# Performance work log

Hardware: AMD Instinct MI355X
Metric: run time of the kernel (lower is better)

Reference implementation:

```python
import jax, jax.numpy as jnp
import numpy as np

N, D, C = 4096, 512, 64
MARGIN = 1.0
INF = jnp.float32(1e30)


def setup_inputs() -> dict:
    key = jax.random.key(0)
    k1, k2 = jax.random.split(key)
    embeddings = jax.random.normal(k1, (N, D), dtype=jnp.float32)
    targets = jax.random.randint(k2, (N,), 0, C)
    return {"embeddings": embeddings, "targets": targets}


def _triplet_loss(embeddings, targets, margin=MARGIN):
    # Squared pairwise distances [N, N] (differentiable, used for the loss)
    sq_norms = jnp.sum(embeddings * embeddings, axis=1)
    sq_dist = jnp.maximum(
        sq_norms[:, None] + sq_norms[None, :] - 2.0 * (embeddings @ embeddings.T), 0.0
    )
    # Euclidean distances for mining only (index selection is non-differentiable in torch)
    dist = jnp.sqrt(jax.lax.stop_gradient(sq_dist))

    same = targets[:, None] == targets[None, :]  # [N, N] same-label mask

    # Hardest negative per anchor: argmax_k (d_ap - d_ak + margin) == argmin_k d_ak over negatives
    neg_dist = jnp.where(same, INF, dist)
    n_idx = jnp.argmin(neg_dist, axis=1)   # [N] hardest negative index per anchor
    min_neg = jnp.min(neg_dist, axis=1)    # [N] its euclidean distance

    idx = jnp.arange(dist.shape[0])
    # anchor-positive pairs: same label, a < p (torch.combinations on sorted indices)
    pair_mask = same & (idx[:, None] < idx[None, :])
    # triplet kept only if mined loss (euclidean) strictly positive
    valid = pair_mask & (dist - min_neg[:, None] + margin > 0)

    ap_sq = sq_dist                         # [N, N] squared anchor-positive distances
    an_sq = sq_dist[idx, n_idx]             # [N]   squared anchor-hard-negative distances
    losses = jax.nn.relu(ap_sq - an_sq[:, None] + margin)

    cnt = jnp.sum(valid)
    denom = jnp.maximum(cnt, 1).astype(losses.dtype)
    loss = jnp.sum(jnp.where(valid, losses, 0.0)) / denom

    correct = jnp.sum(valid & (ap_sq < an_sq[:, None]))
    accuracy = correct.astype(jnp.float32) / jnp.maximum(cnt, 1).astype(jnp.float32)
    return loss, accuracy


def reference(embeddings, targets):
    return _triplet_loss(embeddings, targets)
```

## Files before the change

kernel.cpp:

```cpp
#include <hip/hip_runtime.h>

#define N 4096
#define D 512
#define MARGIN 1.0f
#define TILE 64
#define BK 64
#define SKB 144
#define NTILES (N / TILE)
#define NTRI (NTILES * (NTILES + 1) / 2)
#define FINF 3.0e38f

#define NSLOT 64
#define SLOTW 16

typedef __attribute__((ext_vector_type(8))) short short8;
typedef __attribute__((ext_vector_type(4))) float floatx4;

__device__ __forceinline__ unsigned short f2bf(float f) {
  unsigned int u = __float_as_uint(f);
  u += 0x7FFFu + ((u >> 16) & 1u);
  return (unsigned short)(u >> 16);
}

__global__ void init_kernel(unsigned int* __restrict__ an_sq_bits, unsigned int* __restrict__ accs) {
  int i = blockIdx.x * 256 + threadIdx.x;
  if (i < N) an_sq_bits[i] = 0x7F800000u;
  if (i < NSLOT * SLOTW) accs[i] = 0u;
}

__global__ __launch_bounds__(256) void prep_kernel(const float* __restrict__ E,
                                                   unsigned short* __restrict__ Ebf,
                                                   float* __restrict__ norms) {
  const int row = blockIdx.x;
  const int tid = threadIdx.x;
  const float2 v = reinterpret_cast<const float2*>(E + (size_t)row * D)[tid];
  float s = v.x * v.x + v.y * v.y;
  unsigned int packed = ((unsigned int)f2bf(v.y) << 16) | (unsigned int)f2bf(v.x);
  reinterpret_cast<unsigned int*>(Ebf + (size_t)row * D)[tid] = packed;
  for (int off = 32; off > 0; off >>= 1) s += __shfl_down(s, off);
  __shared__ float wsum[4];
  if ((tid & 63) == 0) wsum[tid >> 6] = s;
  __syncthreads();
  if (tid == 0) norms[row] = wsum[0] + wsum[1] + wsum[2] + wsum[3];
}

__global__ __launch_bounds__(256, 6) void gemm_min_kernel(const unsigned short* __restrict__ Ebf,
                                                          const float* __restrict__ norms,
                                                          const int* __restrict__ targets,
                                                          unsigned int* __restrict__ an_sq_bits) {
  const int u = blockIdx.x;
  int i = (int)((sqrtf(8.0f * (float)u + 1.0f) - 1.0f) * 0.5f);
  while ((i + 1) * (i + 2) / 2 <= u) ++i;
  while (i * (i + 1) / 2 > u) --i;
  const int tm = u - i * (i + 1) / 2;
  const int tn = i;

  __shared__ alignas(16) unsigned char As[TILE * SKB];
  __shared__ alignas(16) unsigned char Bs[TILE * SKB];
  __shared__ float s_rmin[2][TILE];
  __shared__ float s_cmin[2][TILE];

  const int tid = threadIdx.x;
  const int wave = tid >> 6, lane = tid & 63;
  const int quad = lane >> 4, l16 = lane & 15;
  const int wr = wave >> 1, wc = wave & 1;
  const int rowBase = tm * TILE, colBase = tn * TILE;

  floatx4 acc[2][2];
#pragma unroll
  for (int a = 0; a < 2; a++)
#pragma unroll
    for (int b = 0; b < 2; b++) acc[a][b] = (floatx4){0.f, 0.f, 0.f, 0.f};

  for (int k0 = 0; k0 < D; k0 += BK) {
#pragma unroll
    for (int s = tid; s < TILE * 8; s += 256) {
      const int r = s >> 3, q = s & 7;
      const uint4 va = *reinterpret_cast<const uint4*>(&Ebf[(size_t)(rowBase + r) * D + k0 + q * 8]);
      *reinterpret_cast<uint4*>(&As[r * SKB + q * 16]) = va;
      const uint4 vb = *reinterpret_cast<const uint4*>(&Ebf[(size_t)(colBase + r) * D + k0 + q * 8]);
      *reinterpret_cast<uint4*>(&Bs[r * SKB + q * 16]) = vb;
    }
    __syncthreads();
#pragma unroll
    for (int ks = 0; ks < 2; ks++) {
      short8 af[2], bf[2];
#pragma unroll
      for (int s = 0; s < 2; s++) {
        af[s] = *reinterpret_cast<const short8*>(&As[(wr * 32 + s * 16 + l16) * SKB + ks * 64 + quad * 16]);
        bf[s] = *reinterpret_cast<const short8*>(&Bs[(wc * 32 + s * 16 + l16) * SKB + ks * 64 + quad * 16]);
      }
#pragma unroll
      for (int sm = 0; sm < 2; sm++)
#pragma unroll
        for (int sn = 0; sn < 2; sn++)
          acc[sm][sn] = __builtin_amdgcn_mfma_f32_16x16x32_bf16(af[sm], bf[sn], acc[sm][sn], 0, 0, 0);
    }
    __syncthreads();
  }

  int tcol[2];
  float ncol[2];
#pragma unroll
  for (int sn = 0; sn < 2; sn++) {
    const int gc = colBase + wc * 32 + sn * 16 + l16;
    tcol[sn] = targets[gc];
    ncol[sn] = norms[gc];
  }
  float colmin[2] = {FINF, FINF};
#pragma unroll
  for (int sm = 0; sm < 2; sm++) {
#pragma unroll
    for (int r = 0; r < 4; r++) {
      const int rloc = wr * 32 + sm * 16 + quad * 4 + r;
      const int grow = rowBase + rloc;
      const int trow = targets[grow];
      const float nrow = norms[grow];
      float rowmin = FINF;
#pragma unroll
      for (int sn = 0; sn < 2; sn++) {
        const float sq = fmaxf(nrow + ncol[sn] - 2.0f * acc[sm][sn][r], 0.0f);
        if (tcol[sn] != trow) {
          rowmin = fminf(rowmin, sq);
          colmin[sn] = fminf(colmin[sn], sq);
        }
      }
#pragma unroll
      for (int off = 1; off < 16; off <<= 1) rowmin = fminf(rowmin, __shfl_xor(rowmin, off));
      if (l16 == 0) s_rmin[wc][rloc] = rowmin;
    }
  }
#pragma unroll
  for (int sn = 0; sn < 2; sn++) {
    float cm = colmin[sn];
    cm = fminf(cm, __shfl_xor(cm, 16));
    cm = fminf(cm, __shfl_xor(cm, 32));
    if (quad == 0) s_cmin[wr][wc * 32 + sn * 16 + l16] = cm;
  }
  __syncthreads();
  if (tid < TILE) {
    const float m = fminf(s_rmin[0][tid], s_rmin[1][tid]);
    if (m < FINF) atomicMin(&an_sq_bits[rowBase + tid], __float_as_uint(m));
  } else if (tid < 2 * TILE) {
    const int c = tid - TILE;
    const float m = fminf(s_cmin[0][c], s_cmin[1][c]);
    if (m < FINF) atomicMin(&an_sq_bits[colBase + c], __float_as_uint(m));
  }
}

__global__ __launch_bounds__(256) void loss_kernel(const float* __restrict__ E,
                                                   const int* __restrict__ targets,
                                                   const float* __restrict__ norms,
                                                   const unsigned int* __restrict__ an_sq_bits,
                                                   float* __restrict__ accs) {
  const int i = blockIdx.x;
  const int tid = threadIdx.x, wave = tid >> 6, lane = tid & 63;
  __shared__ int list[512];
  __shared__ int lcount;
  __shared__ float s_sum[4];
  __shared__ unsigned int s_cnt[4], s_cor[4];
  if (tid == 0) lcount = 0;
  __syncthreads();
  const int ti = targets[i];
  for (int j = i + 1 + tid; j < N; j += 256) {
    if (targets[j] == ti) {
      int p = atomicAdd(&lcount, 1);
      if (p < 512) list[p] = j;
    }
  }
  float ei[8];
#pragma unroll
  for (int k = 0; k < 8; k++) ei[k] = E[(size_t)i * D + k * 64 + lane];
  __syncthreads();
  const int nm = min(lcount, 512);
  const float an_sq = __uint_as_float(an_sq_bits[i]);
  const float min_neg = sqrtf(an_sq);
  const float ni = norms[i];
  float bsum = 0.f;
  unsigned int bcnt = 0, bcor = 0;
  for (int m = wave * 2; m < nm; m += 8) {
    const int j0 = list[m];
    const bool has1 = (m + 1) < nm;
    const int j1 = has1 ? list[m + 1] : j0;
    float d0 = 0.f, d1 = 0.f;
#pragma unroll
    for (int k = 0; k < 8; k++) {
      d0 += ei[k] * E[(size_t)j0 * D + k * 64 + lane];
      d1 += ei[k] * E[(size_t)j1 * D + k * 64 + lane];
    }
#pragma unroll
    for (int off = 32; off > 0; off >>= 1) {
      d0 += __shfl_down(d0, off);
      d1 += __shfl_down(d1, off);
    }
    if (lane == 0) {
      {
        const float sq = fmaxf(ni + norms[j0] - 2.0f * d0, 0.0f);
        if (sqrtf(sq) - min_neg + MARGIN > 0.0f) {
          bcnt++;
          bsum += fmaxf(sq - an_sq + MARGIN, 0.0f);
          if (sq < an_sq) bcor++;
        }
      }
      if (has1) {
        const float sq = fmaxf(ni + norms[j1] - 2.0f * d1, 0.0f);
        if (sqrtf(sq) - min_neg + MARGIN > 0.0f) {
          bcnt++;
          bsum += fmaxf(sq - an_sq + MARGIN, 0.0f);
          if (sq < an_sq) bcor++;
        }
      }
    }
  }
  if (lane == 0) {
    s_sum[wave] = bsum;
    s_cnt[wave] = bcnt;
    s_cor[wave] = bcor;
  }
  __syncthreads();
  if (tid == 0) {
    const float tsum = s_sum[0] + s_sum[1] + s_sum[2] + s_sum[3];
    const unsigned int tcnt = s_cnt[0] + s_cnt[1] + s_cnt[2] + s_cnt[3];
    const unsigned int tcor = s_cor[0] + s_cor[1] + s_cor[2] + s_cor[3];
    if (tcnt != 0) {
      float* slot = accs + (size_t)(i & (NSLOT - 1)) * SLOTW;
      atomicAdd(&slot[0], tsum);
      atomicAdd((unsigned int*)&slot[1], tcnt);
      atomicAdd((unsigned int*)&slot[2], tcor);
    }
  }
}

__global__ void finalize_kernel(const float* __restrict__ accs, float* __restrict__ out) {
  const int lane = threadIdx.x;
  float sum = accs[(size_t)lane * SLOTW + 0];
  unsigned int cnt = ((const unsigned int*)accs)[(size_t)lane * SLOTW + 1];
  unsigned int cor = ((const unsigned int*)accs)[(size_t)lane * SLOTW + 2];
  for (int off = 32; off > 0; off >>= 1) {
    sum += __shfl_down(sum, off);
    cnt += __shfl_down(cnt, off);
    cor += __shfl_down(cor, off);
  }
  if (lane == 0) {
    const float denom = (float)(cnt > 0u ? cnt : 1u);
    out[0] = sum / denom;
    out[1] = (float)cor / denom;
  }
}

extern "C" void kernel_launch(void* const* d_in, const int* in_sizes, int n_in,
                              void* d_out, int out_size, void* d_ws, size_t ws_size,
                              hipStream_t stream) {
  const float* E = (const float*)d_in[0];
  const int* targets = (const int*)d_in[1];
  float* out = (float*)d_out;
  char* ws = (char*)d_ws;
  unsigned short* Ebf = (unsigned short*)ws;
  float* norms = (float*)(ws + (size_t)N * D * 2);
  unsigned int* an_sq = (unsigned int*)(ws + (size_t)N * D * 2 + N * 4);
  float* accs = (float*)(ws + (size_t)N * D * 2 + (size_t)N * 8);

  init_kernel<<<dim3((N + 255) / 256), dim3(256), 0, stream>>>(an_sq, (unsigned int*)accs);
  prep_kernel<<<dim3(N), dim3(256), 0, stream>>>(E, Ebf, norms);
  gemm_min_kernel<<<dim3(NTRI), dim3(256), 0, stream>>>(Ebf, norms, targets, an_sq);
  loss_kernel<<<dim3(N), dim3(256), 0, stream>>>(E, targets, norms, an_sq, accs);
  finalize_kernel<<<1, 64, 0, stream>>>(accs, out);
}
```

Before: 114.2 us.

## Bucket samples by class and compute positive-pair distances with per-class MFMA tiles

A prep block now builds per-class member lists, and the loss kernel runs one block per class instead of one per anchor. Each block computes intra-class Gram tiles with bf16 MFMA over the upper-triangular 16x16 tile pairs, replacing the per-anchor scan over all N labels and the fp32 dot products. The init kernel is folded into prep, and gemm occupancy bounds are raised from 6 to 8 waves. Class size is capped at MAXM=112, so larger classes would be silently truncated. Positive distances now use bf16 instead of fp32, which may flip borderline validity decisions.

```diff
diff --git a/kernel.cpp b/kernel.cpp
--- a/kernel.cpp
+++ b/kernel.cpp
@@ -2,6 +2,7 @@
 
 #define N 4096
 #define D 512
+#define C 64
 #define MARGIN 1.0f
 #define TILE 64
 #define BK 64
@@ -9,6 +10,7 @@
 #define NTILES (N / TILE)
 #define NTRI (NTILES * (NTILES + 1) / 2)
 #define FINF 3.0e38f
+#define MAXM 112
 
 #define NSLOT 64
 #define SLOTW 16
@@ -22,17 +24,39 @@
   return (unsigned short)(u >> 16);
 }
 
-__global__ void init_kernel(unsigned int* __restrict__ an_sq_bits, unsigned int* __restrict__ accs) {
-  int i = blockIdx.x * 256 + threadIdx.x;
-  if (i < N) an_sq_bits[i] = 0x7F800000u;
-  if (i < NSLOT * SLOTW) accs[i] = 0u;
-}
-
 __global__ __launch_bounds__(256) void prep_kernel(const float* __restrict__ E,
+                                                   const int* __restrict__ targets,
                                                    unsigned short* __restrict__ Ebf,
-                                                   float* __restrict__ norms) {
+                                                   float* __restrict__ norms,
+                                                   unsigned int* __restrict__ an_sq_bits,
+                                                   int* __restrict__ cls_mem,
+                                                   int* __restrict__ cls_off) {
   const int row = blockIdx.x;
   const int tid = threadIdx.x;
+  if (row == N) {
+    __shared__ unsigned int cnt[C];
+    __shared__ unsigned int base[C];
+    if (tid < C) cnt[tid] = 0;
+    __syncthreads();
+    for (int i = tid; i < N; i += 256) atomicAdd(&cnt[targets[i]], 1);
+    __syncthreads();
+    if (tid == 0) {
+      unsigned int s = 0;
+      for (int c = 0; c < C; c++) { base[c] = s; s += cnt[c]; }
+    }
+    __syncthreads();
+    if (tid < C) cnt[tid] = base[tid];
+    __syncthreads();
+    for (int i = tid; i < N; i += 256) {
+      const int c = targets[i];
+      const unsigned int p = atomicAdd(&cnt[c], 1);
+      cls_mem[p] = i;
+    }
+    if (tid < C) cls_off[tid] = (int)base[tid];
+    if (tid == 0) cls_off[C] = N;
+    return;
+  }
+  if (row < 16) an_sq_bits[row * 256 + tid] = 0x7F800000u;
   const float2 v = reinterpret_cast<const float2*>(E + (size_t)row * D)[tid];
   float s = v.x * v.x + v.y * v.y;
   unsigned int packed = ((unsigned int)f2bf(v.y) << 16) | (unsigned int)f2bf(v.x);
@@ -44,7 +68,7 @@
   if (tid == 0) norms[row] = wsum[0] + wsum[1] + wsum[2] + wsum[3];
 }
 
-__global__ __launch_bounds__(256, 6) void gemm_min_kernel(const unsigned short* __restrict__ Ebf,
+__global__ __launch_bounds__(256, 8) void gemm_min_kernel(const unsigned short* __restrict__ Ebf,
                                                           const float* __restrict__ norms,
                                                           const int* __restrict__ targets,
                                                           unsigned int* __restrict__ an_sq_bits) {
@@ -148,86 +172,105 @@
   }
 }
 
-__global__ __launch_bounds__(256) void loss_kernel(const float* __restrict__ E,
-                                                   const int* __restrict__ targets,
+__global__ __launch_bounds__(256) void loss_kernel(const unsigned short* __restrict__ Ebf,
                                                    const float* __restrict__ norms,
                                                    const unsigned int* __restrict__ an_sq_bits,
+                                                   const int* __restrict__ cls_mem,
+                                                   const int* __restrict__ cls_off,
                                                    float* __restrict__ accs) {
-  const int i = blockIdx.x;
+  const int c = blockIdx.x;
   const int tid = threadIdx.x, wave = tid >> 6, lane = tid & 63;
-  __shared__ int list[512];
-  __shared__ int lcount;
+  const int quad = lane >> 4, l16 = lane & 15;
+  const int o = cls_off[c];
+  const int s_c = min(cls_off[c + 1] - o, MAXM);
+
+  __shared__ alignas(16) unsigned char S[MAXM * SKB];
+  __shared__ int l_mem[MAXM];
+  __shared__ float l_norm[MAXM];
+  __shared__ float l_an[MAXM];
+  __shared__ signed char pti[28], ptj[28];
   __shared__ float s_sum[4];
   __shared__ unsigned int s_cnt[4], s_cor[4];
-  if (tid == 0) lcount = 0;
+
+  if (tid < s_c) {
+    const int m = cls_mem[o + tid];
+    l_mem[tid] = m;
+    l_norm[tid] = norms[m];
+    l_an[tid] = __uint_as_float(an_sq_bits[m]);
+  }
+  const int nt = (s_c + 15) >> 4;
+  const int npairs = nt * (nt + 1) / 2;
+  if (tid == 0) {
+    int w = 0;
+    for (int ti = 0; ti < nt; ti++)
+      for (int tj = ti; tj < nt; tj++) { pti[w] = (signed char)ti; ptj[w] = (signed char)tj; w++; }
+  }
   __syncthreads();
-  const int ti = targets[i];
-  for (int j = i + 1 + tid; j < N; j += 256) {
-    if (targets[j] == ti) {
-      int p = atomicAdd(&lcount, 1);
-      if (p < 512) list[p] = j;
-    }
-  }
-  float ei[8];
-#pragma unroll
-  for (int k = 0; k < 8; k++) ei[k] = E[(size_t)i * D + k * 64 + lane];
-  __syncthreads();
-  const int nm = min(lcount, 512);
-  const float an_sq = __uint_as_float(an_sq_bits[i]);
-  const float min_neg = sqrtf(an_sq);
-  const float ni = norms[i];
+
+  floatx4 pacc[7];
+#pragma unroll
+  for (int pp = 0; pp < 7; pp++) pacc[pp] = (floatx4){0.f, 0.f, 0.f, 0.f};
+
+  for (int k0 = 0; k0 < D; k0 += BK) {
+    for (int s = tid; s < s_c * 8; s += 256) {
+      const int r = s >> 3, q = s & 7;
+      *reinterpret_cast<uint4*>(&S[r * SKB + q * 16]) =
+          *reinterpret_cast<const uint4*>(&Ebf[(size_t)l_mem[r] * D + k0 + q * 8]);
+    }
+    __syncthreads();
+#pragma unroll
+    for (int pp = 0; pp < 7; pp++) {
+      const int p = wave + 4 * pp;
+      if (p < npairs) {
+        const int ti = pti[p], tj = ptj[p];
+#pragma unroll
+        for (int ks = 0; ks < 2; ks++) {
+          const short8 af = *reinterpret_cast<const short8*>(&S[(ti * 16 + l16) * SKB + ks * 64 + quad * 16]);
+          const short8 bf = *reinterpret_cast<const short8*>(&S[(tj * 16 + l16) * SKB + ks * 64 + quad * 16]);
+          pacc[pp] = __builtin_amdgcn_mfma_f32_16x16x32_bf16(af, bf, pacc[pp], 0, 0, 0);
+        }
+      }
+    }
+    __syncthreads();
+  }
+
   float bsum = 0.f;
   unsigned int bcnt = 0, bcor = 0;
-  for (int m = wave * 2; m < nm; m += 8) {
-    const int j0 = list[m];
-    const bool has1 = (m + 1) < nm;
-    const int j1 = has1 ? list[m + 1] : j0;
-    float d0 = 0.f, d1 = 0.f;
-#pragma unroll
-    for (int k = 0; k < 8; k++) {
-      d0 += ei[k] * E[(size_t)j0 * D + k * 64 + lane];
-      d1 += ei[k] * E[(size_t)j1 * D + k * 64 + lane];
-    }
-#pragma unroll
-    for (int off = 32; off > 0; off >>= 1) {
-      d0 += __shfl_down(d0, off);
-      d1 += __shfl_down(d1, off);
-    }
-    if (lane == 0) {
-      {
-        const float sq = fmaxf(ni + norms[j0] - 2.0f * d0, 0.0f);
-        if (sqrtf(sq) - min_neg + MARGIN > 0.0f) {
-          bcnt++;
-          bsum += fmaxf(sq - an_sq + MARGIN, 0.0f);
-          if (sq < an_sq) bcor++;
+#pragma unroll
+  for (int pp = 0; pp < 7; pp++) {
+    const int p = wave + 4 * pp;
+    if (p < npairs) {
+      const int ti = pti[p], tj = ptj[p];
+#pragma unroll
+      for (int r = 0; r < 4; r++) {
+        const int i_loc = ti * 16 + quad * 4 + r;
+        const int j_loc = tj * 16 + l16;
+        if (i_loc < s_c && j_loc < s_c && (ti < tj || i_loc < j_loc)) {
+          const int oi = l_mem[i_loc], oj = l_mem[j_loc];
+          const float sq = fmaxf(l_norm[i_loc] + l_norm[j_loc] - 2.0f * pacc[pp][r], 0.0f);
+          const float an = (oi < oj) ? l_an[i_loc] : l_an[j_loc];
+          if (sqrtf(sq) - sqrtf(an) + MARGIN > 0.0f) {
+            bcnt++;
+            bsum += fmaxf(sq - an + MARGIN, 0.0f);
+            if (sq < an) bcor++;
+          }
         }
       }
-      if (has1) {
-        const float sq = fmaxf(ni + norms[j1] - 2.0f * d1, 0.0f);
-        if (sqrtf(sq) - min_neg + MARGIN > 0.0f) {
-          bcnt++;
-          bsum += fmaxf(sq - an_sq + MARGIN, 0.0f);
-          if (sq < an_sq) bcor++;
-        }
-      }
-    }
-  }
-  if (lane == 0) {
-    s_sum[wave] = bsum;
-    s_cnt[wave] = bcnt;
-    s_cor[wave] = bcor;
-  }
+    }
+  }
+#pragma unroll
+  for (int off = 32; off > 0; off >>= 1) {
+    bsum += __shfl_down(bsum, off);
+    bcnt += __shfl_down(bcnt, off);
+    bcor += __shfl_down(bcor, off);
+  }
+  if (lane == 0) { s_sum[wave] = bsum; s_cnt[wave] = bcnt; s_cor[wave] = bcor; }
   __syncthreads();
   if (tid == 0) {
-    const float tsum = s_sum[0] + s_sum[1] + s_sum[2] + s_sum[3];
-    const unsigned int tcnt = s_cnt[0] + s_cnt[1] + s_cnt[2] + s_cnt[3];
-    const unsigned int tcor = s_cor[0] + s_cor[1] + s_cor[2] + s_cor[3];
-    if (tcnt != 0) {
-      float* slot = accs + (size_t)(i & (NSLOT - 1)) * SLOTW;
-      atomicAdd(&slot[0], tsum);
-      atomicAdd((unsigned int*)&slot[1], tcnt);
-      atomicAdd((unsigned int*)&slot[2], tcor);
-    }
+    float* slot = accs + (size_t)c * SLOTW;
+    slot[0] = s_sum[0] + s_sum[1] + s_sum[2] + s_sum[3];
+    ((unsigned int*)slot)[1] = s_cnt[0] + s_cnt[1] + s_cnt[2] + s_cnt[3];
+    ((unsigned int*)slot)[2] = s_cor[0] + s_cor[1] + s_cor[2] + s_cor[3];
   }
 }
 
@@ -255,14 +298,16 @@
   const int* targets = (const int*)d_in[1];
   float* out = (float*)d_out;
   char* ws = (char*)d_ws;
-  unsigned short* Ebf = (unsigned short*)ws;
-  float* norms = (float*)(ws + (size_t)N * D * 2);
-  unsigned int* an_sq = (unsigned int*)(ws + (size_t)N * D * 2 + N * 4);
-  float* accs = (float*)(ws + (size_t)N * D * 2 + (size_t)N * 8);
-
-  init_kernel<<<dim3((N + 255) / 256), dim3(256), 0, stream>>>(an_sq, (unsigned int*)accs);
-  prep_kernel<<<dim3(N), dim3(256), 0, stream>>>(E, Ebf, norms);
+  size_t off = 0;
+  unsigned short* Ebf = (unsigned short*)(ws + off); off += (size_t)N * D * 2;
+  float* norms = (float*)(ws + off); off += (size_t)N * 4;
+  unsigned int* an_sq = (unsigned int*)(ws + off); off += (size_t)N * 4;
+  float* accs = (float*)(ws + off); off += (size_t)NSLOT * SLOTW * 4;
+  int* cls_mem = (int*)(ws + off); off += (size_t)N * 4;
+  int* cls_off = (int*)(ws + off);
+
+  prep_kernel<<<dim3(N + 1), dim3(256), 0, stream>>>(E, targets, Ebf, norms, an_sq, cls_mem, cls_off);
   gemm_min_kernel<<<dim3(NTRI), dim3(256), 0, stream>>>(Ebf, norms, targets, an_sq);
-  loss_kernel<<<dim3(N), dim3(256), 0, stream>>>(E, targets, norms, an_sq, accs);
+  loss_kernel<<<dim3(C), dim3(256), 0, stream>>>(Ebf, norms, an_sq, cls_mem, cls_off, accs);
   finalize_kernel<<<1, 64, 0, stream>>>(accs, out);
 }
```

After: 113.5 us. About the same (-0.7%).
